# Optimization experiments

Measured on AMD Instinct MI355X. Metric: run time of the kernel, lower is better.

Reference implementation:

```python
import jax, jax.numpy as jnp
import numpy as np

OUT_DIM = 512
NUM_SAMPLES = 4096
NUM_ATTRIBUTES = 128

def setup_inputs() -> dict:
    key = jax.random.key(0)
    k1, k2 = jax.random.split(key)
    x = jax.random.normal(k1, (1, NUM_SAMPLES), dtype=jnp.float32)
    # LSH projection weights, scaled by 0.15 as in the torch module
    weights = jax.random.normal(k2, (OUT_DIM, NUM_SAMPLES, NUM_ATTRIBUTES), dtype=jnp.float32) * 0.15
    return {"x": x, "weights": weights}

def reference(x, weights):
    # Original (per i): ret[i] = sum_a (x[0] @ weights[i])[a]
    # Fused: single contraction over samples s and attributes a.
    # x: [1, S]; weights: [O, S, A] -> ret: [O]
    return jnp.einsum('s,osa->o', x[0], weights)
```

## Files before the change

### kernel.cpp

```cpp
#include <hip/hip_runtime.h>


#define OUT_DIM 512
#define NS 4096
#define NA 128
#define SLICES 8
#define BLOCK 256

__global__ __launch_bounds__(BLOCK) void lsh_reduce_kernel(
        const float* __restrict__ x,
        const float* __restrict__ w,
        float* __restrict__ out) {
    __shared__ float xs[NS];
    __shared__ float part[BLOCK / 64];

    const float4* x4 = (const float4*)x;
    for (int i = threadIdx.x; i < NS / 4; i += BLOCK) {
        float4 v = x4[i];
        xs[i * 4 + 0] = v.x;
        xs[i * 4 + 1] = v.y;
        xs[i * 4 + 2] = v.z;
        xs[i * 4 + 3] = v.w;
    }
    __syncthreads();

    const int o     = blockIdx.x >> 3;
    const int slice = blockIdx.x & (SLICES - 1);
    const float4* w4 = (const float4*)(w + (size_t)o * (NS * NA));
    const int base = slice * 16384;

    float acc = 0.0f;
    #pragma unroll 8
    for (int i = 0; i < 64; ++i) {
        const int idx4 = base + i * BLOCK + (int)threadIdx.x;
        float4 v = w4[idx4];
        const int s = idx4 >> 5;
        acc += (v.x + v.y + v.z + v.w) * xs[s];
    }

    #pragma unroll
    for (int off = 32; off > 0; off >>= 1)
        acc += __shfl_down(acc, off, 64);

    const int lane = threadIdx.x & 63;
    const int wave = threadIdx.x >> 6;
    if (lane == 0) part[wave] = acc;
    __syncthreads();
    if (threadIdx.x == 0) {
        float t = part[0] + part[1] + part[2] + part[3];
        atomicAdd(out + o, t);
    }
}

__global__ void lsh_zero_out(float* __restrict__ out) {
    out[blockIdx.x * BLOCK + threadIdx.x] = 0.0f;
}

extern "C" void kernel_launch(void* const* d_in, const int* in_sizes, int n_in,
                              void* d_out, int out_size, void* d_ws, size_t ws_size,
                              hipStream_t stream) {
    const float* x = (const float*)d_in[0];
    const float* w = (const float*)d_in[1];
    float* out = (float*)d_out;

    lsh_zero_out<<<OUT_DIM / BLOCK, BLOCK, 0, stream>>>(out);
    lsh_reduce_kernel<<<OUT_DIM * SLICES, BLOCK, 0, stream>>>(x, w, out);
}
```

Baseline: 1.310 ms.

## Use one 1024-thread block per output and drop the zeroing kernel and atomics

Each output row is now reduced by a single 1024-thread block instead of eight 256-thread slices combined with atomicAdd. This removes the separate zero-init kernel launch and the atomics, and the block writes its result directly. The grid drops to 512 blocks, which may reduce how well the memory-bound stream of weight loads is spread across CUs and kept in flight.

```diff
diff --git a/kernel.cpp b/kernel.cpp
--- a/kernel.cpp
+++ b/kernel.cpp
@@ -4,8 +4,11 @@
 #define OUT_DIM 512
 #define NS 4096
 #define NA 128
-#define SLICES 8
-#define BLOCK 256
+#define BLOCK 1024
+#define F4_PER_O (NS * NA / 4)
+#define ITERS (F4_PER_O / BLOCK)
+
+typedef float f32x4 __attribute__((ext_vector_type(4)));
 
 __global__ __launch_bounds__(BLOCK) void lsh_reduce_kernel(
         const float* __restrict__ x,
@@ -14,28 +17,18 @@
     __shared__ float xs[NS];
     __shared__ float part[BLOCK / 64];
 
-    const float4* x4 = (const float4*)x;
-    for (int i = threadIdx.x; i < NS / 4; i += BLOCK) {
-        float4 v = x4[i];
-        xs[i * 4 + 0] = v.x;
-        xs[i * 4 + 1] = v.y;
-        xs[i * 4 + 2] = v.z;
-        xs[i * 4 + 3] = v.w;
-    }
+    ((f32x4*)xs)[threadIdx.x] = ((const f32x4*)x)[threadIdx.x];
     __syncthreads();
 
-    const int o     = blockIdx.x >> 3;
-    const int slice = blockIdx.x & (SLICES - 1);
-    const float4* w4 = (const float4*)(w + (size_t)o * (NS * NA));
-    const int base = slice * 16384;
+    const int o = blockIdx.x;
+    const f32x4* __restrict__ w4 = (const f32x4*)(w + (size_t)o * (NS * NA));
 
     float acc = 0.0f;
     #pragma unroll 8
-    for (int i = 0; i < 64; ++i) {
-        const int idx4 = base + i * BLOCK + (int)threadIdx.x;
-        float4 v = w4[idx4];
-        const int s = idx4 >> 5;
-        acc += (v.x + v.y + v.z + v.w) * xs[s];
+    for (int i = 0; i < ITERS; ++i) {
+        const int idx4 = i * BLOCK + (int)threadIdx.x;
+        f32x4 v = w4[idx4];
+        acc += (v.x + v.y + v.z + v.w) * xs[idx4 >> 5];
     }
 
     #pragma unroll
@@ -47,13 +40,11 @@
     if (lane == 0) part[wave] = acc;
     __syncthreads();
     if (threadIdx.x == 0) {
-        float t = part[0] + part[1] + part[2] + part[3];
-        atomicAdd(out + o, t);
+        float t = 0.0f;
+        #pragma unroll
+        for (int i = 0; i < BLOCK / 64; ++i) t += part[i];
+        out[o] = t;
     }
-}
-
-__global__ void lsh_zero_out(float* __restrict__ out) {
-    out[blockIdx.x * BLOCK + threadIdx.x] = 0.0f;
 }
 
 extern "C" void kernel_launch(void* const* d_in, const int* in_sizes, int n_in,
@@ -62,7 +53,5 @@
     const float* x = (const float*)d_in[0];
     const float* w = (const float*)d_in[1];
     float* out = (float*)d_out;
-
-    lsh_zero_out<<<OUT_DIM / BLOCK, BLOCK, 0, stream>>>(out);
-    lsh_reduce_kernel<<<OUT_DIM * SLICES, BLOCK, 0, stream>>>(x, w, out);
+    lsh_reduce_kernel<<<OUT_DIM, BLOCK, 0, stream>>>(x, w, out);
 }
```

After: 1.300 ms. Within noise of the previous version (-0.8%).
